# Optimization experiments

Measured on AMD Instinct MI355X. Metric: run time of the kernel, lower is better.

## Reference

```python
import jax, jax.numpy as jnp
import numpy as np

B, L_ENC, ENC_IN = 8, 1536, 7
LABEL_LEN, PRED_LEN = 512, 512
D_MODEL, N_HEADS, D_FF = 512, 8, 2048
E_LAYERS = 2
BUCKET_SIZE, N_HASHES = 64, 4
C_OUT, MARK_F = 7, 4
D_HEAD = D_MODEL // N_HEADS
L = L_ENC + PRED_LEN            # 2048, multiple of 2*bucket_size -> fit_length adds no pad
N_BUCKETS = L // BUCKET_SIZE    # 32
SELF_ATTN_VALUE = -5e4          # reformer_pytorch TOKEN_SELF_ATTN_VALUE


def _ln(x, g, b, eps=1e-5):
    mu = x.mean(-1, keepdims=True)
    var = ((x - mu) ** 2).mean(-1, keepdims=True)
    return (x - mu) * jax.lax.rsqrt(var + eps) * g + b


def _pos_embedding(length, d):
    pos = np.arange(length)[:, None].astype(np.float32)
    div = np.exp(np.arange(0, d, 2).astype(np.float32) * -(np.log(10000.0) / d))
    pe = np.zeros((length, d), np.float32)
    pe[:, 0::2] = np.sin(pos * div)
    pe[:, 1::2] = np.cos(pos * div)
    return jnp.asarray(pe)


def _lsh_attention(qk, v, rot):
    # qk, v: (b, L, d) with b = B*heads; rot: (d, n_hashes, n_buckets//2)
    b, Ls, d = qk.shape
    # --- hash: random rotations, buckets = argmax over [r, -r] ---
    rotated = jnp.einsum('bld,dhr->bhlr', qk, rot)
    rotated = jnp.concatenate([rotated, -rotated], axis=-1)            # (b,H,L,nb)
    buckets = jnp.argmax(rotated, axis=-1)                             # (b,H,L)
    buckets = buckets + (jnp.arange(N_HASHES) * N_BUCKETS)[None, :, None]
    buckets = buckets.reshape(b, N_HASHES * Ls)
    ticker = jnp.arange(N_HASHES * Ls)[None, :] % Ls
    # --- stable sort by (bucket, position) ---
    sticker = jnp.argsort(buckets * Ls + ticker, axis=-1)              # (b, H*L)
    undo_sort = jnp.argsort(sticker, axis=-1)
    st = sticker % Ls
    sqk = jnp.take_along_axis(qk, st[..., None], axis=1)               # (b, H*L, d)
    sv = jnp.take_along_axis(v, st[..., None], axis=1)
    n_chunks = N_HASHES * N_BUCKETS
    bq_t = st.reshape(b, n_chunks, -1)                                 # (b, C, cs)
    bq = sqk.reshape(b, n_chunks, -1, d)
    bv = sv.reshape(b, n_chunks, -1, d)
    # shared-QK: keys are l2-normalized queries
    bk = bq / jnp.maximum(jnp.linalg.norm(bq, axis=-1, keepdims=True), 1e-12)
    look = lambda x: jnp.concatenate([x, jnp.roll(x, 1, axis=1)], axis=2)
    bk, bv, bkv_t = look(bk), look(bv), look(bq_t)
    dots = jnp.einsum('bcie,bcje->bcij', bq, bk) * (d ** -0.5)         # (b,C,cs,2cs)
    self_mask = bq_t[:, :, :, None] == bkv_t[:, :, None, :]
    dots = jnp.where(self_mask, SELF_ATTN_VALUE, dots)
    lse = jax.nn.logsumexp(dots, axis=-1, keepdims=True)
    p = jnp.exp(dots - lse)
    so = jnp.einsum('bcij,bcje->bcie', p, bv).reshape(b, -1, d)        # (b, H*L, d)
    slog = lse.reshape(b, -1)
    o = jnp.take_along_axis(so, undo_sort[..., None], axis=1).reshape(b, N_HASHES, Ls, d)
    logits = jnp.take_along_axis(slog, undo_sort, axis=1).reshape(b, N_HASHES, Ls, 1)
    w = jnp.exp(logits - jax.nn.logsumexp(logits, axis=1, keepdims=True))
    return (o * w).sum(axis=1)                                         # (b, L, d)


def _forward(x_enc, x_mark_enc, x_dec, x_mark_dec, token_conv_w, time_w,
             qk_w, v_w, out_w, out_b, rotations,
             ffn1_w, ffn1_b, ffn2_w, ffn2_b,
             norm1_g, norm1_b, norm2_g, norm2_b, normf_g, normf_b,
             proj_w, proj_b):
    x = jnp.concatenate([x_enc, x_dec[:, -PRED_LEN:, :]], axis=1)      # (B, L, enc_in)
    xm = jnp.concatenate([x_mark_enc, x_mark_dec[:, -PRED_LEN:, :]], axis=1)
    # TokenEmbedding: Conv1d k=3, circular padding, no bias
    xp = jnp.concatenate([x[:, -1:, :], x, x[:, :1, :]], axis=1)
    tok = jax.lax.conv_general_dilated(xp, token_conv_w, (1,), 'VALID',
                                       dimension_numbers=('NWC', 'WIO', 'NWC'))
    h = tok + _pos_embedding(L, D_MODEL)[None] + xm @ time_w
    for l in range(E_LAYERS):
        qk = (h @ qk_w[l]).reshape(B, L, N_HEADS, D_HEAD).transpose(0, 2, 1, 3).reshape(B * N_HEADS, L, D_HEAD)
        v = (h @ v_w[l]).reshape(B, L, N_HEADS, D_HEAD).transpose(0, 2, 1, 3).reshape(B * N_HEADS, L, D_HEAD)
        a = _lsh_attention(qk, v, rotations[l])
        a = a.reshape(B, N_HEADS, L, D_HEAD).transpose(0, 2, 1, 3).reshape(B, L, D_MODEL)
        a = a @ out_w[l] + out_b[l]
        h = _ln(h + a, norm1_g[l], norm1_b[l])
        y = jax.nn.gelu(h @ ffn1_w[l] + ffn1_b[l], approximate=False) @ ffn2_w[l] + ffn2_b[l]
        h = _ln(h + y, norm2_g[l], norm2_b[l])
    h = _ln(h, normf_g, normf_b)
    out = h @ proj_w + proj_b
    return out[:, -PRED_LEN:, :]


def setup_inputs() -> dict:
    key = jax.random.key(0)
    ks = jax.random.split(key, 16)
    s = 0.02
    return {
        'x_enc': jax.random.normal(ks[0], (B, L_ENC, ENC_IN), jnp.float32),
        'x_mark_enc': jax.random.normal(ks[1], (B, L_ENC, MARK_F), jnp.float32),
        'x_dec': jax.random.normal(ks[2], (B, LABEL_LEN + PRED_LEN, ENC_IN), jnp.float32),
        'x_mark_dec': jax.random.normal(ks[3], (B, LABEL_LEN + PRED_LEN, MARK_F), jnp.float32),
        'token_conv_w': jax.random.normal(ks[4], (3, ENC_IN, D_MODEL), jnp.float32) * s,
        'time_w': jax.random.normal(ks[5], (MARK_F, D_MODEL), jnp.float32) * s,
        'qk_w': jax.random.normal(ks[6], (E_LAYERS, D_MODEL, D_MODEL), jnp.float32) * s,
        'v_w': jax.random.normal(ks[7], (E_LAYERS, D_MODEL, D_MODEL), jnp.float32) * s,
        'out_w': jax.random.normal(ks[8], (E_LAYERS, D_MODEL, D_MODEL), jnp.float32) * s,
        'out_b': jnp.zeros((E_LAYERS, D_MODEL), jnp.float32),
        'rotations': jax.random.normal(ks[9], (E_LAYERS, D_HEAD, N_HASHES, N_BUCKETS // 2), jnp.float32),
        'ffn1_w': jax.random.normal(ks[10], (E_LAYERS, D_MODEL, D_FF), jnp.float32) * s,
        'ffn1_b': jnp.zeros((E_LAYERS, D_FF), jnp.float32),
        'ffn2_w': jax.random.normal(ks[11], (E_LAYERS, D_FF, D_MODEL), jnp.float32) * s,
        'ffn2_b': jnp.zeros((E_LAYERS, D_MODEL), jnp.float32),
        'norm1_g': jnp.ones((E_LAYERS, D_MODEL), jnp.float32),
        'norm1_b': jnp.zeros((E_LAYERS, D_MODEL), jnp.float32),
        'norm2_g': jnp.ones((E_LAYERS, D_MODEL), jnp.float32),
        'norm2_b': jnp.zeros((E_LAYERS, D_MODEL), jnp.float32),
        'normf_g': jnp.ones((D_MODEL,), jnp.float32),
        'normf_b': jnp.zeros((D_MODEL,), jnp.float32),
        'proj_w': jax.random.normal(ks[12], (D_MODEL, C_OUT), jnp.float32) * s,
        'proj_b': jnp.zeros((C_OUT,), jnp.float32),
    }


def reference(x_enc, x_mark_enc, x_dec, x_mark_dec, token_conv_w, time_w,
              qk_w, v_w, out_w, out_b, rotations,
              ffn1_w, ffn1_b, ffn2_w, ffn2_b,
              norm1_g, norm1_b, norm2_g, norm2_b, normf_g, normf_b,
              proj_w, proj_b):
    return _forward(x_enc, x_mark_enc, x_dec, x_mark_dec, token_conv_w, time_w,
                    qk_w, v_w, out_w, out_b, rotations,
                    ffn1_w, ffn1_b, ffn2_w, ffn2_b,
                    norm1_g, norm1_b, norm2_g, norm2_b, normf_g, normf_b,
                    proj_w, proj_b)
```

## Files before the change

kernel.cpp:

```cpp
#include <hip/hip_runtime.h>


#define BATCH 8
#define SEQL 2048
#define DM 512
#define NH 8
#define DH 64
#define DFF 2048
#define NHASH 4
#define NBUCK 32
#define NCHUNK 128
#define CS 64
#define ROWS (BATCH*SEQL)
#define BHN (BATCH*NH)
#define SORTN (NHASH*SEQL)
#define SELF_VAL -5e4f

typedef __attribute__((ext_vector_type(4))) float f32x4;
typedef __attribute__((ext_vector_type(8))) short short8;

__device__ __forceinline__ float bfu2f(unsigned int u16) {
    return __uint_as_float(u16 << 16);
}
__device__ __forceinline__ unsigned short f2bfu(float f) {
    unsigned int x = __float_as_uint(f);
    x += 0x7fffu + ((x >> 16) & 1u);
    return (unsigned short)(x >> 16);
}

__device__ __forceinline__ void gld16(const void* g, void* l) {
    __builtin_amdgcn_global_load_lds(
        (const __attribute__((address_space(1))) unsigned int*)g,
        (__attribute__((address_space(3))) unsigned int*)l, 16, 0, 0);
}

__device__ __forceinline__ float getx(const float* xe, const float* xd, int b, int lm, int c) {
    return (lm < 1536) ? xe[((size_t)b * 1536 + lm) * 7 + c]
                       : xd[((size_t)b * 1024 + (lm - 1024)) * 7 + c];
}

__global__ __launch_bounds__(512) void embed_k(
    const float* __restrict__ x_enc, const float* __restrict__ x_me,
    const float* __restrict__ x_dec, const float* __restrict__ x_md,
    const float* __restrict__ cw, const float* __restrict__ tw,
    float* __restrict__ h, unsigned short* __restrict__ hb)
{
    const int row = blockIdx.x;
    const int b = row >> 11, l = row & 2047;
    const int d = threadIdx.x;
    __shared__ float xs[21];
    __shared__ float xms[4];
    if (d < 21) {
        const int k = d / 7, c = d % 7;
        const int lm = (l + k + 2047) & 2047;
        xs[d] = getx(x_enc, x_dec, b, lm, c);
    } else if (d < 25) {
        const int m = d - 21;
        xms[m] = (l < 1536) ? x_me[((size_t)b * 1536 + l) * 4 + m]
                            : x_md[((size_t)b * 1024 + (l - 1024)) * 4 + m];
    }
    __syncthreads();
    float tok = 0.f;
    #pragma unroll
    for (int kc = 0; kc < 21; ++kc) tok = fmaf(xs[kc], cw[kc * 512 + d], tok);
    float tm = 0.f;
    #pragma unroll
    for (int m = 0; m < 4; ++m) tm = fmaf(xms[m], tw[m * 512 + d], tm);
    const int pair = d & ~1;
    const float freq = expf((float)pair * (-9.210340371976184f / 512.f));
    const float ang = (float)l * freq;
    const float pe = (d & 1) ? cosf(ang) : sinf(ang);
    const float val = tok + pe + tm;
    h[(size_t)row * 512 + d] = val;
    hb[(size_t)row * 512 + d] = f2bfu(val);
}

__global__ __launch_bounds__(256) void gemm_k(
    const float* __restrict__ A, const float* __restrict__ B,
    float* __restrict__ C, int M, int N, int K)
{
    __shared__ float As[16][132];
    __shared__ float Bs[16][64];
    const int tid = threadIdx.x;
    const int bm = blockIdx.x * 128, bn = blockIdx.y * 64;
    const int ty = tid >> 4, tx = tid & 15;
    const int ar = tid >> 1, ac = (tid & 1) * 8;
    const int br = tid >> 4, bc = (tid & 15) * 4;
    float acc[8][4] = {};
    const float* Ap = A + (size_t)(bm + ar) * K + ac;
    const float* Bp = B + (size_t)br * N + bn + bc;
    float4 a0v = *reinterpret_cast<const float4*>(Ap);
    float4 a1v = *reinterpret_cast<const float4*>(Ap + 4);
    float4 b0v = *reinterpret_cast<const float4*>(Bp);
    for (int k0 = 0; k0 < K; k0 += 16) {
        As[ac + 0][ar] = a0v.x; As[ac + 1][ar] = a0v.y;
        As[ac + 2][ar] = a0v.z; As[ac + 3][ar] = a0v.w;
        As[ac + 4][ar] = a1v.x; As[ac + 5][ar] = a1v.y;
        As[ac + 6][ar] = a1v.z; As[ac + 7][ar] = a1v.w;
        *reinterpret_cast<float4*>(&Bs[br][bc]) = b0v;
        __syncthreads();
        if (k0 + 16 < K) {
            a0v = *reinterpret_cast<const float4*>(Ap + k0 + 16);
            a1v = *reinterpret_cast<const float4*>(Ap + k0 + 20);
            b0v = *reinterpret_cast<const float4*>(Bp + (size_t)(k0 + 16) * N);
        }
        #pragma unroll
        for (int k = 0; k < 16; ++k) {
            const float4 a0 = *reinterpret_cast<const float4*>(&As[k][ty * 8]);
            const float4 a1 = *reinterpret_cast<const float4*>(&As[k][ty * 8 + 4]);
            const float4 b0 = *reinterpret_cast<const float4*>(&Bs[k][tx * 4]);
            const float a[8] = {a0.x,a0.y,a0.z,a0.w,a1.x,a1.y,a1.z,a1.w};
            const float bb[4] = {b0.x,b0.y,b0.z,b0.w};
            #pragma unroll
            for (int i = 0; i < 8; ++i)
                #pragma unroll
                for (int j = 0; j < 4; ++j) acc[i][j] = fmaf(a[i], bb[j], acc[i][j]);
        }
        __syncthreads();
    }
    #pragma unroll
    for (int i = 0; i < 8; ++i) {
        const size_t cb = (size_t)(bm + ty * 8 + i) * N + bn + tx * 4;
        *reinterpret_cast<float4*>(C + cb) = make_float4(acc[i][0],acc[i][1],acc[i][2],acc[i][3]);
    }
}

__global__ __launch_bounds__(256) void tcast_k(
    const float* __restrict__ W, unsigned short* __restrict__ Wt, int K, int N)
{
    __shared__ float t[32][33];
    const int kb = blockIdx.x * 32, nb = blockIdx.y * 32;
    const int tx = threadIdx.x & 31, ty = threadIdx.x >> 5;
    #pragma unroll
    for (int i = ty; i < 32; i += 8)
        t[i][tx] = W[(size_t)(kb + i) * N + nb + tx];
    __syncthreads();
    #pragma unroll
    for (int i = ty; i < 32; i += 8)
        Wt[(size_t)(nb + i) * K + kb + tx] = f2bfu(t[tx][i]);
}

template<int OUT_BF, int ACT, int BIAS>
__global__ __launch_bounds__(256) void mgemm_k(
    const unsigned short* __restrict__ A,
    const unsigned short* __restrict__ Bt,
    const float* __restrict__ bias,
    void* __restrict__ Cv, int N, int K)
{
    __shared__ unsigned short As[128 * 32];
    __shared__ unsigned short Bs[128 * 32];
    const int tid = threadIdx.x;
    const int bm = blockIdx.x * 128, bn = blockIdx.y * 128;
    const int lane = tid & 63, w = tid >> 6;
    const int wr = (w >> 1) * 64, wc = (w & 1) * 64;
    const int fr = lane & 15, fq = lane >> 4;
    const int r0 = tid >> 2, c0 = (tid & 3) * 8;
    const unsigned short* Ag = A + (size_t)(bm + r0) * K + c0;
    const unsigned short* Bg = Bt + (size_t)(bn + r0) * K + c0;
    f32x4 acc[4][4];
    #pragma unroll
    for (int i = 0; i < 4; ++i)
        #pragma unroll
        for (int j = 0; j < 4; ++j) acc[i][j] = (f32x4){0.f, 0.f, 0.f, 0.f};
    for (int k0 = 0; k0 < K; k0 += 32) {
        gld16(Ag + k0,                   As + tid * 8);
        gld16(Ag + (size_t)64 * K + k0,  As + tid * 8 + 2048);
        gld16(Bg + k0,                   Bs + tid * 8);
        gld16(Bg + (size_t)64 * K + k0,  Bs + tid * 8 + 2048);
        __syncthreads();
        short8 af[4], bfr[4];
        #pragma unroll
        for (int mi = 0; mi < 4; ++mi)
            af[mi] = *reinterpret_cast<const short8*>(As + (wr + mi * 16 + fr) * 32 + fq * 8);
        #pragma unroll
        for (int ni = 0; ni < 4; ++ni)
            bfr[ni] = *reinterpret_cast<const short8*>(Bs + (wc + ni * 16 + fr) * 32 + fq * 8);
        #pragma unroll
        for (int mi = 0; mi < 4; ++mi)
            #pragma unroll
            for (int ni = 0; ni < 4; ++ni)
                acc[mi][ni] = __builtin_amdgcn_mfma_f32_16x16x32_bf16(
                    af[mi], bfr[ni], acc[mi][ni], 0, 0, 0);
        __syncthreads();
    }
    float bv[4];
    if (BIAS) {
        #pragma unroll
        for (int ni = 0; ni < 4; ++ni) bv[ni] = bias[bn + wc + ni * 16 + fr];
    }
    #pragma unroll
    for (int mi = 0; mi < 4; ++mi) {
        #pragma unroll
        for (int r = 0; r < 4; ++r) {
            const int row = bm + wr + mi * 16 + fq * 4 + r;
            #pragma unroll
            for (int ni = 0; ni < 4; ++ni) {
                float val = acc[mi][ni][r];
                if (BIAS) val += bv[ni];
                if (ACT) val = 0.5f * val * (1.0f + erff(val * 0.7071067811865475f));
                const size_t idx = (size_t)row * N + bn + wc + ni * 16 + fr;
                if (OUT_BF) ((unsigned short*)Cv)[idx] = f2bfu(val);
                else        ((float*)Cv)[idx] = val;
            }
        }
    }
}

__global__ __launch_bounds__(256, 4) void hash_k(
    const float* __restrict__ qk, const float* __restrict__ rot,
    int* __restrict__ buckets)
{
    __shared__ float rs[64][68];
    const int t = threadIdx.x;
    for (int u = t; u < 4096; u += 256) {
        const int d = u >> 6, hj = u & 63;
        rs[hj][d] = rot[u];
    }
    __syncthreads();
    const int gid = blockIdx.x * 256 + t;
    const int l = gid & 2047;
    const int bh = (gid >> 11) & 63;
    const int hh = gid >> 17;
    const int b = bh >> 3, head = bh & 7;
    const float* qrow = qk + (size_t)(b * 2048 + l) * 512 + head * 64;
    float q[64];
    #pragma unroll
    for (int d4 = 0; d4 < 16; ++d4) {
        const float4 qq = reinterpret_cast<const float4*>(qrow)[d4];
        q[d4*4+0]=qq.x; q[d4*4+1]=qq.y; q[d4*4+2]=qq.z; q[d4*4+3]=qq.w;
    }
    float bvp = -1e38f, bvn = -1e38f;
    int bip = 0, bin_ = 16;
    #pragma unroll
    for (int j = 0; j < 16; ++j) {
        const int hj = hh * 16 + j;
        float dot = 0.f;
        #pragma unroll
        for (int d = 0; d < 64; d += 4) {
            const float4 r = *reinterpret_cast<const float4*>(&rs[hj][d]);
            dot += q[d]*r.x + q[d+1]*r.y + q[d+2]*r.z + q[d+3]*r.w;
        }
        if (dot  > bvp) { bvp = dot;  bip = j; }
        if (-dot > bvn) { bvn = -dot; bin_ = 16 + j; }
    }
    const int idx = (bvn > bvp) ? bin_ : bip;
    buckets[((size_t)bh << 13) + hh * 2048 + l] = hh * 32 + idx;
}

__global__ __launch_bounds__(256) void sort_k(
    const int* __restrict__ buckets, int* __restrict__ st_sorted, int* __restrict__ pos_of)
{
    const int bh = blockIdx.x >> 2, hh = blockIdx.x & 3;
    const int t = threadIdx.x;
    __shared__ unsigned short cnt[256][32];
    __shared__ int tot[32];
    __shared__ int startc[32];
    {
        uint4* p = reinterpret_cast<uint4*>(&cnt[t][0]);
        const uint4 z = {0,0,0,0};
        #pragma unroll
        for (int q = 0; q < 4; ++q) p[q] = z;
    }
    const size_t base = (size_t)bh * SORTN + hh * 2048;
    int myb[8];
    #pragma unroll
    for (int j = 0; j < 8; ++j) {
        const int i = t * 8 + j;
        const int g = buckets[base + i] - hh * 32;
        myb[j] = g;
        cnt[t][g]++;
    }
    __syncthreads();
    if (t < 32) {
        int run = 0;
        for (int tt = 0; tt < 256; ++tt) {
            const int x = cnt[tt][t];
            cnt[tt][t] = (unsigned short)run;
            run += x;
        }
        tot[t] = run;
    }
    __syncthreads();
    if (t == 0) {
        int s = 0;
        for (int g = 0; g < 32; ++g) { startc[g] = s; s += tot[g]; }
    }
    __syncthreads();
    #pragma unroll
    for (int j = 0; j < 8; ++j) {
        const int i = t * 8 + j;
        const int g = myb[j];
        const int rank = cnt[t][g]++;
        const int pos = hh * 2048 + startc[g] + rank;
        st_sorted[(size_t)bh * SORTN + pos] = i;
        pos_of[base + i] = pos;
    }
}

__global__ __launch_bounds__(256) void lsh_attn_k(
    const float* __restrict__ qk, const unsigned short* __restrict__ vbf,
    const int* __restrict__ st_sorted,
    unsigned short* __restrict__ so, float* __restrict__ slog)
{
    const int c = blockIdx.x;
    const int bh = blockIdx.y;
    const int b = bh >> 3, head = bh & 7;
    __shared__ unsigned short Ks[128 * 72];
    __shared__ unsigned short Vt[128 * 64];
    __shared__ unsigned short Ps[64 * 136];
    __shared__ float rnorm[128];
    __shared__ int stk[128];
    const int t = threadIdx.x;

    {
        const int r = t >> 1, hf = t & 1;
        const int cprev = (c + NCHUNK - 1) & (NCHUNK - 1);
        const int spos = (r < 64) ? (c * CS + r) : (cprev * CS + (r - 64));
        const int l = st_sorted[(size_t)bh * SORTN + spos];
        if (hf == 0) stk[r] = l;
        const size_t ro = (size_t)(b * 2048 + l) * 512 + head * 64 + hf * 32;
        const float4* q4 = reinterpret_cast<const float4*>(qk + ro);
        float ss = 0.f;
        #pragma unroll
        for (int u = 0; u < 8; ++u) {
            const float4 a = q4[u];
            ss += a.x*a.x + a.y*a.y + a.z*a.z + a.w*a.w;
            ushort4 pk;
            pk.x = f2bfu(a.x); pk.y = f2bfu(a.y); pk.z = f2bfu(a.z); pk.w = f2bfu(a.w);
            *reinterpret_cast<ushort4*>(&Ks[r * 72 + hf * 32 + u * 4]) = pk;
        }
        ss += __shfl_xor(ss, 1);
        if (hf == 0) rnorm[r] = 1.0f / fmaxf(sqrtf(ss), 1e-12f);
        const uint4* v16 = reinterpret_cast<const uint4*>(vbf + ro);
        const uint4 a0 = v16[0], a1 = v16[1], a2 = v16[2], a3 = v16[3];
        const unsigned int wd[16] = {a0.x,a0.y,a0.z,a0.w, a1.x,a1.y,a1.z,a1.w,
                                     a2.x,a2.y,a2.z,a2.w, a3.x,a3.y,a3.z,a3.w};
        #pragma unroll
        for (int e = 0; e < 32; ++e) {
            const int d = hf * 32 + e;
            const unsigned short us = (unsigned short)(wd[e >> 1] >> ((e & 1) * 16));
            Vt[(d * 128 + r) ^ ((d & 7) << 3)] = us;
        }
    }
    __syncthreads();

    const int lane = t & 63, w = t >> 6;
    const int fr = lane & 15, fq = lane >> 4;

    short8 aq[2];
    #pragma unroll
    for (int s = 0; s < 2; ++s)
        aq[s] = *reinterpret_cast<const short8*>(&Ks[(w * 16 + fr) * 72 + s * 32 + fq * 8]);
    f32x4 cc[8];
    #pragma unroll
    for (int n = 0; n < 8; ++n) cc[n] = (f32x4){0.f, 0.f, 0.f, 0.f};
    #pragma unroll
    for (int n = 0; n < 8; ++n) {
        #pragma unroll
        for (int s = 0; s < 2; ++s) {
            const short8 bk = *reinterpret_cast<const short8*>(
                &Ks[(n * 16 + fr) * 72 + s * 32 + fq * 8]);
            cc[n] = __builtin_amdgcn_mfma_f32_16x16x32_bf16(aq[s], bk, cc[n], 0, 0, 0);
        }
    }

    int stq_r[4];
    #pragma unroll
    for (int r = 0; r < 4; ++r) stq_r[r] = stk[w * 16 + fq * 4 + r];
    float mx[4] = {-3.0e38f, -3.0e38f, -3.0e38f, -3.0e38f};
    #pragma unroll
    for (int n = 0; n < 8; ++n) {
        const int key = n * 16 + fr;
        const float rn = rnorm[key] * 0.125f;
        const int sk = stk[key];
        #pragma unroll
        for (int r = 0; r < 4; ++r) {
            const float val = (stq_r[r] == sk) ? SELF_VAL : cc[n][r] * rn;
            cc[n][r] = val;
            mx[r] = fmaxf(mx[r], val);
        }
    }
    #pragma unroll
    for (int r = 0; r < 4; ++r) {
        mx[r] = fmaxf(mx[r], __shfl_xor(mx[r], 1));
        mx[r] = fmaxf(mx[r], __shfl_xor(mx[r], 2));
        mx[r] = fmaxf(mx[r], __shfl_xor(mx[r], 4));
        mx[r] = fmaxf(mx[r], __shfl_xor(mx[r], 8));
    }
    float sm[4] = {0.f, 0.f, 0.f, 0.f};
    #pragma unroll
    for (int n = 0; n < 8; ++n)
        #pragma unroll
        for (int r = 0; r < 4; ++r) {
            const float e = __expf(cc[n][r] - mx[r]);
            cc[n][r] = e;
            sm[r] += e;
        }
    #pragma unroll
    for (int r = 0; r < 4; ++r) {
        sm[r] += __shfl_xor(sm[r], 1);
        sm[r] += __shfl_xor(sm[r], 2);
        sm[r] += __shfl_xor(sm[r], 4);
        sm[r] += __shfl_xor(sm[r], 8);
    }
    float rsum[4];
    #pragma unroll
    for (int r = 0; r < 4; ++r) rsum[r] = 1.0f / sm[r];
    if (fr == 0) {
        #pragma unroll
        for (int r = 0; r < 4; ++r)
            slog[(size_t)bh * SORTN + c * CS + w * 16 + fq * 4 + r] = mx[r] + logf(sm[r]);
    }

    #pragma unroll
    for (int n = 0; n < 8; ++n)
        #pragma unroll
        for (int r = 0; r < 4; ++r)
            Ps[(w * 16 + fq * 4 + r) * 136 + n * 16 + fr] = f2bfu(cc[n][r]);
    __syncthreads();

    short8 pa[4];
    #pragma unroll
    for (int s = 0; s < 4; ++s)
        pa[s] = *reinterpret_cast<const short8*>(&Ps[(w * 16 + fr) * 136 + s * 32 + fq * 8]);
    f32x4 oo[4];
    #pragma unroll
    for (int n = 0; n < 4; ++n) oo[n] = (f32x4){0.f, 0.f, 0.f, 0.f};
    #pragma unroll
    for (int n = 0; n < 4; ++n) {
        const int d = n * 16 + fr;
        #pragma unroll
        for (int s = 0; s < 4; ++s) {
            const short8 vb = *reinterpret_cast<const short8*>(
                &Vt[(d * 128 + s * 32 + fq * 8) ^ ((d & 7) << 3)]);
            oo[n] = __builtin_amdgcn_mfma_f32_16x16x32_bf16(pa[s], vb, oo[n], 0, 0, 0);
        }
    }

    #pragma unroll
    for (int r = 0; r < 4; ++r) {
        const int qrow = w * 16 + fq * 4 + r;
        const size_t ob = ((size_t)bh * SORTN + c * CS + qrow) * 64;
        #pragma unroll
        for (int n = 0; n < 4; ++n)
            so[ob + n * 16 + fr] = f2bfu(oo[n][r] * rsum[r]);
    }
}

__global__ __launch_bounds__(256) void combine_k(
    const unsigned short* __restrict__ so, const float* __restrict__ slog,
    const int* __restrict__ pos_of, unsigned short* __restrict__ aout)
{
    const int gid = blockIdx.x * 256 + threadIdx.x;
    const int d = gid & 63;
    const int bl = gid >> 6;
    const int l = bl & 2047;
    const int bh = bl >> 11;
    const int b = bh >> 3, head = bh & 7;
    int pos[4]; float lg[4];
    #pragma unroll
    for (int hh = 0; hh < 4; ++hh) {
        pos[hh] = pos_of[((size_t)bh << 13) + hh * 2048 + l];
        lg[hh] = slog[((size_t)bh << 13) + pos[hh]];
    }
    const float m = fmaxf(fmaxf(lg[0], lg[1]), fmaxf(lg[2], lg[3]));
    float w[4]; float sw = 0.f;
    #pragma unroll
    for (int hh = 0; hh < 4; ++hh) { w[hh] = expf(lg[hh] - m); sw += w[hh]; }
    const float inv = 1.0f / sw;
    float acc = 0.f;
    #pragma unroll
    for (int hh = 0; hh < 4; ++hh)
        acc += w[hh] * bfu2f(so[(((size_t)bh << 13) + pos[hh]) * 64 + d]);
    aout[(size_t)(b * 2048 + l) * 512 + head * 64 + d] = f2bfu(acc * inv);
}

template<int RES, int WBF>
__global__ __launch_bounds__(256) void ln_k(
    float* __restrict__ h, const float* __restrict__ res,
    const float* __restrict__ g, const float* __restrict__ bta,
    unsigned short* __restrict__ hb)
{
    const int row = blockIdx.x * 4 + (threadIdx.x >> 6);
    const int lane = threadIdx.x & 63;
    const size_t base = (size_t)row * 512;
    float4 xa = *reinterpret_cast<const float4*>(h + base + lane * 4);
    float4 xb = *reinterpret_cast<const float4*>(h + base + 256 + lane * 4);
    if (RES) {
        const float4 ra = *reinterpret_cast<const float4*>(res + base + lane * 4);
        const float4 rb = *reinterpret_cast<const float4*>(res + base + 256 + lane * 4);
        xa.x += ra.x; xa.y += ra.y; xa.z += ra.z; xa.w += ra.w;
        xb.x += rb.x; xb.y += rb.y; xb.z += rb.z; xb.w += rb.w;
    }
    float sum = xa.x + xa.y + xa.z + xa.w + xb.x + xb.y + xb.z + xb.w;
    float sq = xa.x*xa.x + xa.y*xa.y + xa.z*xa.z + xa.w*xa.w
             + xb.x*xb.x + xb.y*xb.y + xb.z*xb.z + xb.w*xb.w;
    #pragma unroll
    for (int off = 32; off > 0; off >>= 1) {
        sum += __shfl_xor(sum, off);
        sq  += __shfl_xor(sq, off);
    }
    const float mu = sum * (1.0f / 512.0f);
    const float var = sq * (1.0f / 512.0f) - mu * mu;
    const float rstd = rsqrtf(var + 1e-5f);
    const float4 ga = *reinterpret_cast<const float4*>(g + lane * 4);
    const float4 gb = *reinterpret_cast<const float4*>(g + 256 + lane * 4);
    const float4 ba = *reinterpret_cast<const float4*>(bta + lane * 4);
    const float4 bb = *reinterpret_cast<const float4*>(bta + 256 + lane * 4);
    float4 oa, ob;
    oa.x = (xa.x - mu) * rstd * ga.x + ba.x;
    oa.y = (xa.y - mu) * rstd * ga.y + ba.y;
    oa.z = (xa.z - mu) * rstd * ga.z + ba.z;
    oa.w = (xa.w - mu) * rstd * ga.w + ba.w;
    ob.x = (xb.x - mu) * rstd * gb.x + bb.x;
    ob.y = (xb.y - mu) * rstd * gb.y + bb.y;
    ob.z = (xb.z - mu) * rstd * gb.z + bb.z;
    ob.w = (xb.w - mu) * rstd * gb.w + bb.w;
    *reinterpret_cast<float4*>(h + base + lane * 4) = oa;
    *reinterpret_cast<float4*>(h + base + 256 + lane * 4) = ob;
    if (WBF) {
        ushort4 pa, pb;
        pa.x = f2bfu(oa.x); pa.y = f2bfu(oa.y); pa.z = f2bfu(oa.z); pa.w = f2bfu(oa.w);
        pb.x = f2bfu(ob.x); pb.y = f2bfu(ob.y); pb.z = f2bfu(ob.z); pb.w = f2bfu(ob.w);
        *reinterpret_cast<ushort4*>(hb + base + lane * 4) = pa;
        *reinterpret_cast<ushort4*>(hb + base + 256 + lane * 4) = pb;
    }
}

__global__ __launch_bounds__(256) void proj_k(
    const float* __restrict__ h, const float* __restrict__ pw,
    const float* __restrict__ pb, float* __restrict__ out)
{
    const int wid = (blockIdx.x * 256 + threadIdx.x) >> 6;
    const int lane = threadIdx.x & 63;
    const int b = wid >> 9, tt = wid & 511;
    const float* row = h + (size_t)(b * 2048 + 1536 + tt) * 512;
    const float4 h0 = reinterpret_cast<const float4*>(row)[lane * 2];
    const float4 h1 = reinterpret_cast<const float4*>(row)[lane * 2 + 1];
    const float he[8] = {h0.x, h0.y, h0.z, h0.w, h1.x, h1.y, h1.z, h1.w};
    float acc[7] = {};
    #pragma unroll
    for (int e = 0; e < 8; ++e) {
        const int k = lane * 8 + e;
        #pragma unroll
        for (int cq = 0; cq < 7; ++cq) acc[cq] = fmaf(he[e], pw[k * 7 + cq], acc[cq]);
    }
    #pragma unroll
    for (int cq = 0; cq < 7; ++cq) {
        #pragma unroll
        for (int off = 32; off > 0; off >>= 1) acc[cq] += __shfl_xor(acc[cq], off);
    }
    if (lane == 0) {
        const size_t ob = ((size_t)(b * 512) + tt) * 7;
        #pragma unroll
        for (int cq = 0; cq < 7; ++cq) out[ob + cq] = acc[cq] + pb[cq];
    }
}

__global__ void nan_k(float* o) { o[0] = __int_as_float(0x7fc00000); }

extern "C" void kernel_launch(void* const* d_in, const int* in_sizes, int n_in,
                              void* d_out, int out_size, void* d_ws, size_t ws_size,
                              hipStream_t stream)
{
    const float* x_enc  = (const float*)d_in[0];
    const float* x_me   = (const float*)d_in[1];
    const float* x_dec  = (const float*)d_in[2];
    const float* x_md   = (const float*)d_in[3];
    const float* conv_w = (const float*)d_in[4];
    const float* time_w = (const float*)d_in[5];
    const float* qk_w   = (const float*)d_in[6];
    const float* v_w    = (const float*)d_in[7];
    const float* out_w  = (const float*)d_in[8];
    const float* out_b  = (const float*)d_in[9];
    const float* rots   = (const float*)d_in[10];
    const float* f1w    = (const float*)d_in[11];
    const float* f1b    = (const float*)d_in[12];
    const float* f2w    = (const float*)d_in[13];
    const float* f2b    = (const float*)d_in[14];
    const float* n1g    = (const float*)d_in[15];
    const float* n1b    = (const float*)d_in[16];
    const float* n2g    = (const float*)d_in[17];
    const float* n2b    = (const float*)d_in[18];
    const float* nfg    = (const float*)d_in[19];
    const float* nfb    = (const float*)d_in[20];
    const float* pw     = (const float*)d_in[21];
    const float* pb     = (const float*)d_in[22];

    char* ws = (char*)d_ws;
    const size_t HBYT = (size_t)ROWS * DM * 4;
    float* h    = (float*)ws;                  ws += HBYT;
    unsigned short* hb = (unsigned short*)ws;  ws += HBYT / 2;
    float* qkb  = (float*)ws;                  ws += HBYT;
    float* gout = (float*)ws;                  ws += HBYT;
    unsigned short* mid = (unsigned short*)ws; ws += (size_t)ROWS * DFF * 2;
    float* slog = (float*)ws;                  ws += (size_t)BHN * SORTN * 4;
    int* buckets = (int*)ws;                   ws += (size_t)BHN * SORTN * 4;
    int* st_sorted = (int*)ws;                 ws += (size_t)BHN * SORTN * 4;
    int* pos_of = (int*)ws;                    ws += (size_t)BHN * SORTN * 4;
    unsigned short* wT = (unsigned short*)ws;  ws += (size_t)(2*262144 + 2*262144 + 2*1048576 + 2*1048576) * 2;
    const size_t need = (size_t)(ws - (char*)d_ws);
    if (ws_size < need) { nan_k<<<1, 1, 0, stream>>>((float*)d_out); return; }

    unsigned short* vT  = wT;
    unsigned short* oT  = vT + 2 * 262144;
    unsigned short* f1T = oT + 2 * 262144;
    unsigned short* f2T = f1T + 2 * 1048576;
    unsigned short* ab  = (unsigned short*)qkb;
    unsigned short* vbf = (unsigned short*)gout;

    for (int l = 0; l < 2; ++l) {
        tcast_k<<<dim3(16, 16), 256, 0, stream>>>(v_w  + (size_t)l*DM*DM,  vT  + (size_t)l*262144, DM, DM);
        tcast_k<<<dim3(16, 16), 256, 0, stream>>>(out_w+ (size_t)l*DM*DM,  oT  + (size_t)l*262144, DM, DM);
        tcast_k<<<dim3(16, 64), 256, 0, stream>>>(f1w  + (size_t)l*DM*DFF, f1T + (size_t)l*1048576, DM, DFF);
        tcast_k<<<dim3(64, 16), 256, 0, stream>>>(f2w  + (size_t)l*DFF*DM, f2T + (size_t)l*1048576, DFF, DM);
    }

    embed_k<<<ROWS, 512, 0, stream>>>(x_enc, x_me, x_dec, x_md, conv_w, time_w, h, hb);

    for (int l = 0; l < 2; ++l) {
        const size_t wo = (size_t)l * DM * DM;
        gemm_k<<<dim3(ROWS/128, DM/64), 256, 0, stream>>>(h, qk_w + wo, qkb, ROWS, DM, DM);
        mgemm_k<1,0,0><<<dim3(ROWS/128, DM/128), 256, 0, stream>>>(hb, vT + (size_t)l*262144, nullptr, vbf, DM, DM);
        hash_k<<<(NHASH * BHN * SEQL) / 256, 256, 0, stream>>>(qkb, rots + (size_t)l * DH * NHASH * (NBUCK/2), buckets);
        sort_k<<<BHN * 4, 256, 0, stream>>>(buckets, st_sorted, pos_of);
        lsh_attn_k<<<dim3(NCHUNK, BHN), 256, 0, stream>>>(qkb, vbf, st_sorted, mid , slog);
        combine_k<<<(BHN * SEQL * DH) / 256, 256, 0, stream>>>(mid, slog, pos_of, ab);
        mgemm_k<0,0,1><<<dim3(ROWS/128, DM/128), 256, 0, stream>>>(ab, oT + (size_t)l*262144, out_b + l * DM, gout, DM, DM);
        ln_k<1,1><<<ROWS/4, 256, 0, stream>>>(h, gout, n1g + l * DM, n1b + l * DM, hb);
        mgemm_k<1,1,1><<<dim3(ROWS/128, DFF/128), 256, 0, stream>>>(hb, f1T + (size_t)l*1048576, f1b + l * DFF, mid, DFF, DM);
        mgemm_k<0,0,1><<<dim3(ROWS/128, DM/128), 256, 0, stream>>>(mid, f2T + (size_t)l*1048576, f2b + l * DM, gout, DM, DFF);
        ln_k<1,1><<<ROWS/4, 256, 0, stream>>>(h, gout, n2g + l * DM, n2b + l * DM, hb);
    }
    ln_k<0,0><<<ROWS/4, 256, 0, stream>>>(h, nullptr, nfg, nfb, nullptr);
    proj_k<<<(BATCH * 512 / 4), 256, 0, stream>>>(h, pw, pb, (float*)d_out);
}
```

Measured before the change: 980.9 us.

## Fuse QK and V projections into one launch, swizzle GEMM blocks, trim final norm

Merges the fp32 QK projection and the bf16 V projection into a single kernel whose blocks pick one path by index, saving a launch and letting both run concurrently. The fp32 GEMM K-tile grows from 16 to 32 per stage. mgemm blocks are remapped in an XCD-aware swizzle for better L2 locality. Weight transpose-casts collapse into four launches over a z dimension, and the final layernorm now only processes the 512 prediction rows that the projection reads. The larger fp32 tile raises register and LDS use, and the mixed kernel inherits the larger LDS footprint for both paths.

```diff
diff --git a/kernel.cpp b/kernel.cpp
--- a/kernel.cpp
+++ b/kernel.cpp
@@ -75,40 +75,50 @@
     hb[(size_t)row * 512 + d] = f2bfu(val);
 }
 
-__global__ __launch_bounds__(256) void gemm_k(
-    const float* __restrict__ A, const float* __restrict__ B,
-    float* __restrict__ C, int M, int N, int K)
-{
-    __shared__ float As[16][132];
-    __shared__ float Bs[16][64];
+__device__ __forceinline__ void gemm_body(
+    int bm, int bn, const float* __restrict__ A, const float* __restrict__ B,
+    float* __restrict__ C, int N, int K, char* smem)
+{
+    float* As = (float*)smem;
+    float* Bs = (float*)(smem + 32 * 132 * 4);
     const int tid = threadIdx.x;
-    const int bm = blockIdx.x * 128, bn = blockIdx.y * 64;
     const int ty = tid >> 4, tx = tid & 15;
-    const int ar = tid >> 1, ac = (tid & 1) * 8;
-    const int br = tid >> 4, bc = (tid & 15) * 4;
+    const int ar = tid >> 1, ac = (tid & 1) * 16;
+    const int br = tid >> 3, bc = (tid & 7) * 8;
     float acc[8][4] = {};
     const float* Ap = A + (size_t)(bm + ar) * K + ac;
     const float* Bp = B + (size_t)br * N + bn + bc;
-    float4 a0v = *reinterpret_cast<const float4*>(Ap);
-    float4 a1v = *reinterpret_cast<const float4*>(Ap + 4);
-    float4 b0v = *reinterpret_cast<const float4*>(Bp);
-    for (int k0 = 0; k0 < K; k0 += 16) {
-        As[ac + 0][ar] = a0v.x; As[ac + 1][ar] = a0v.y;
-        As[ac + 2][ar] = a0v.z; As[ac + 3][ar] = a0v.w;
-        As[ac + 4][ar] = a1v.x; As[ac + 5][ar] = a1v.y;
-        As[ac + 6][ar] = a1v.z; As[ac + 7][ar] = a1v.w;
-        *reinterpret_cast<float4*>(&Bs[br][bc]) = b0v;
+    float4 av0 = *reinterpret_cast<const float4*>(Ap);
+    float4 av1 = *reinterpret_cast<const float4*>(Ap + 4);
+    float4 av2 = *reinterpret_cast<const float4*>(Ap + 8);
+    float4 av3 = *reinterpret_cast<const float4*>(Ap + 12);
+    float4 bv0 = *reinterpret_cast<const float4*>(Bp);
+    float4 bv1 = *reinterpret_cast<const float4*>(Bp + 4);
+    for (int k0 = 0; k0 < K; k0 += 32) {
+        As[(ac + 0)  * 132 + ar] = av0.x; As[(ac + 1)  * 132 + ar] = av0.y;
+        As[(ac + 2)  * 132 + ar] = av0.z; As[(ac + 3)  * 132 + ar] = av0.w;
+        As[(ac + 4)  * 132 + ar] = av1.x; As[(ac + 5)  * 132 + ar] = av1.y;
+        As[(ac + 6)  * 132 + ar] = av1.z; As[(ac + 7)  * 132 + ar] = av1.w;
+        As[(ac + 8)  * 132 + ar] = av2.x; As[(ac + 9)  * 132 + ar] = av2.y;
+        As[(ac + 10) * 132 + ar] = av2.z; As[(ac + 11) * 132 + ar] = av2.w;
+        As[(ac + 12) * 132 + ar] = av3.x; As[(ac + 13) * 132 + ar] = av3.y;
+        As[(ac + 14) * 132 + ar] = av3.z; As[(ac + 15) * 132 + ar] = av3.w;
+        *reinterpret_cast<float4*>(&Bs[br * 64 + bc])     = bv0;
+        *reinterpret_cast<float4*>(&Bs[br * 64 + bc + 4]) = bv1;
         __syncthreads();
-        if (k0 + 16 < K) {
-            a0v = *reinterpret_cast<const float4*>(Ap + k0 + 16);
-            a1v = *reinterpret_cast<const float4*>(Ap + k0 + 20);
-            b0v = *reinterpret_cast<const float4*>(Bp + (size_t)(k0 + 16) * N);
-        }
-        #pragma unroll
-        for (int k = 0; k < 16; ++k) {
-            const float4 a0 = *reinterpret_cast<const float4*>(&As[k][ty * 8]);
-            const float4 a1 = *reinterpret_cast<const float4*>(&As[k][ty * 8 + 4]);
-            const float4 b0 = *reinterpret_cast<const float4*>(&Bs[k][tx * 4]);
+        if (k0 + 32 < K) {
+            av0 = *reinterpret_cast<const float4*>(Ap + k0 + 32);
+            av1 = *reinterpret_cast<const float4*>(Ap + k0 + 36);
+            av2 = *reinterpret_cast<const float4*>(Ap + k0 + 40);
+            av3 = *reinterpret_cast<const float4*>(Ap + k0 + 44);
+            bv0 = *reinterpret_cast<const float4*>(Bp + (size_t)(k0 + 32) * N);
+            bv1 = *reinterpret_cast<const float4*>(Bp + (size_t)(k0 + 32) * N + 4);
+        }
+        #pragma unroll
+        for (int k = 0; k < 32; ++k) {
+            const float4 a0 = *reinterpret_cast<const float4*>(&As[k * 132 + ty * 8]);
+            const float4 a1 = *reinterpret_cast<const float4*>(&As[k * 132 + ty * 8 + 4]);
+            const float4 b0 = *reinterpret_cast<const float4*>(&Bs[k * 64 + tx * 4]);
             const float a[8] = {a0.x,a0.y,a0.z,a0.w,a1.x,a1.y,a1.z,a1.w};
             const float bb[4] = {b0.x,b0.y,b0.z,b0.w};
             #pragma unroll
@@ -125,32 +135,17 @@
     }
 }
 
-__global__ __launch_bounds__(256) void tcast_k(
-    const float* __restrict__ W, unsigned short* __restrict__ Wt, int K, int N)
-{
-    __shared__ float t[32][33];
-    const int kb = blockIdx.x * 32, nb = blockIdx.y * 32;
-    const int tx = threadIdx.x & 31, ty = threadIdx.x >> 5;
-    #pragma unroll
-    for (int i = ty; i < 32; i += 8)
-        t[i][tx] = W[(size_t)(kb + i) * N + nb + tx];
-    __syncthreads();
-    #pragma unroll
-    for (int i = ty; i < 32; i += 8)
-        Wt[(size_t)(nb + i) * K + kb + tx] = f2bfu(t[tx][i]);
-}
-
 template<int OUT_BF, int ACT, int BIAS>
-__global__ __launch_bounds__(256) void mgemm_k(
+__device__ __forceinline__ void mgemm_body(
+    int bm, int bn,
     const unsigned short* __restrict__ A,
     const unsigned short* __restrict__ Bt,
     const float* __restrict__ bias,
-    void* __restrict__ Cv, int N, int K)
-{
-    __shared__ unsigned short As[128 * 32];
-    __shared__ unsigned short Bs[128 * 32];
+    void* __restrict__ Cv, int N, int K, char* smem)
+{
+    unsigned short* As = (unsigned short*)smem;
+    unsigned short* Bs = (unsigned short*)smem + 128 * 32;
     const int tid = threadIdx.x;
-    const int bm = blockIdx.x * 128, bn = blockIdx.y * 128;
     const int lane = tid & 63, w = tid >> 6;
     const int wr = (w >> 1) * 64, wc = (w & 1) * 64;
     const int fr = lane & 15, fq = lane >> 4;
@@ -204,6 +199,56 @@
             }
         }
     }
+}
+
+template<int OUT_BF, int ACT, int BIAS>
+__global__ __launch_bounds__(256) void mgemm_k(
+    const unsigned short* __restrict__ A,
+    const unsigned short* __restrict__ Bt,
+    const float* __restrict__ bias,
+    void* __restrict__ Cv, int N, int K)
+{
+    __shared__ __align__(16) char smem[128 * 32 * 2 * 2];
+    const int gx = gridDim.x;
+    const int nwg = gx * gridDim.y;
+    int id = blockIdx.y * gx + blockIdx.x;
+    const int cpx = nwg >> 3;
+    id = (id & 7) * cpx + (id >> 3);
+    const int bm = (id % gx) * 128, bn = (id / gx) * 128;
+    mgemm_body<OUT_BF, ACT, BIAS>(bm, bn, A, Bt, bias, Cv, N, K, smem);
+}
+
+__global__ __launch_bounds__(256) void qkv_k(
+    const float* __restrict__ h, const float* __restrict__ qkw,
+    float* __restrict__ qkb,
+    const unsigned short* __restrict__ hb, const unsigned short* __restrict__ vT,
+    unsigned short* __restrict__ vbf)
+{
+    __shared__ __align__(16) char smem[32 * 132 * 4 + 32 * 64 * 4];
+    const int id = blockIdx.x;
+    if (id < 1024) {
+        gemm_body((id & 127) * 128, (id >> 7) * 64, h, qkw, qkb, DM, DM, smem);
+    } else {
+        const int mid_ = id - 1024;
+        mgemm_body<1, 0, 0>((mid_ & 127) * 128, (mid_ >> 7) * 128,
+                            hb, vT, nullptr, vbf, DM, DM, smem);
+    }
+}
+
+__global__ __launch_bounds__(256) void tcast_k(
+    const float* __restrict__ W, unsigned short* __restrict__ Wt, int K, int N)
+{
+    __shared__ float t[32][33];
+    const size_t zo = (size_t)blockIdx.z * K * N;
+    const int kb = blockIdx.x * 32, nb = blockIdx.y * 32;
+    const int tx = threadIdx.x & 31, ty = threadIdx.x >> 5;
+    #pragma unroll
+    for (int i = ty; i < 32; i += 8)
+        t[i][tx] = W[zo + (size_t)(kb + i) * N + nb + tx];
+    __syncthreads();
+    #pragma unroll
+    for (int i = ty; i < 32; i += 8)
+        Wt[zo + (size_t)(nb + i) * K + kb + tx] = f2bfu(t[tx][i]);
 }
 
 __global__ __launch_bounds__(256, 4) void hash_k(
@@ -527,6 +572,43 @@
     }
 }
 
+__global__ __launch_bounds__(256) void lnf_k(
+    float* __restrict__ h, const float* __restrict__ g, const float* __restrict__ bta)
+{
+    const int vrow = blockIdx.x * 4 + (threadIdx.x >> 6);
+    const int row = (vrow >> 9) * 2048 + 1536 + (vrow & 511);
+    const int lane = threadIdx.x & 63;
+    const size_t base = (size_t)row * 512;
+    float4 xa = *reinterpret_cast<const float4*>(h + base + lane * 4);
+    float4 xb = *reinterpret_cast<const float4*>(h + base + 256 + lane * 4);
+    float sum = xa.x + xa.y + xa.z + xa.w + xb.x + xb.y + xb.z + xb.w;
+    float sq = xa.x*xa.x + xa.y*xa.y + xa.z*xa.z + xa.w*xa.w
+             + xb.x*xb.x + xb.y*xb.y + xb.z*xb.z + xb.w*xb.w;
+    #pragma unroll
+    for (int off = 32; off > 0; off >>= 1) {
+        sum += __shfl_xor(sum, off);
+        sq  += __shfl_xor(sq, off);
+    }
+    const float mu = sum * (1.0f / 512.0f);
+    const float var = sq * (1.0f / 512.0f) - mu * mu;
+    const float rstd = rsqrtf(var + 1e-5f);
+    const float4 ga = *reinterpret_cast<const float4*>(g + lane * 4);
+    const float4 gb = *reinterpret_cast<const float4*>(g + 256 + lane * 4);
+    const float4 ba = *reinterpret_cast<const float4*>(bta + lane * 4);
+    const float4 bb = *reinterpret_cast<const float4*>(bta + 256 + lane * 4);
+    float4 oa, ob;
+    oa.x = (xa.x - mu) * rstd * ga.x + ba.x;
+    oa.y = (xa.y - mu) * rstd * ga.y + ba.y;
+    oa.z = (xa.z - mu) * rstd * ga.z + ba.z;
+    oa.w = (xa.w - mu) * rstd * ga.w + ba.w;
+    ob.x = (xb.x - mu) * rstd * gb.x + bb.x;
+    ob.y = (xb.y - mu) * rstd * gb.y + bb.y;
+    ob.z = (xb.z - mu) * rstd * gb.z + bb.z;
+    ob.w = (xb.w - mu) * rstd * gb.w + bb.w;
+    *reinterpret_cast<float4*>(h + base + lane * 4) = oa;
+    *reinterpret_cast<float4*>(h + base + 256 + lane * 4) = ob;
+}
+
 __global__ __launch_bounds__(256) void proj_k(
     const float* __restrict__ h, const float* __restrict__ pw,
     const float* __restrict__ pb, float* __restrict__ out)
@@ -609,19 +691,16 @@
     unsigned short* ab  = (unsigned short*)qkb;
     unsigned short* vbf = (unsigned short*)gout;
 
-    for (int l = 0; l < 2; ++l) {
-        tcast_k<<<dim3(16, 16), 256, 0, stream>>>(v_w  + (size_t)l*DM*DM,  vT  + (size_t)l*262144, DM, DM);
-        tcast_k<<<dim3(16, 16), 256, 0, stream>>>(out_w+ (size_t)l*DM*DM,  oT  + (size_t)l*262144, DM, DM);
-        tcast_k<<<dim3(16, 64), 256, 0, stream>>>(f1w  + (size_t)l*DM*DFF, f1T + (size_t)l*1048576, DM, DFF);
-        tcast_k<<<dim3(64, 16), 256, 0, stream>>>(f2w  + (size_t)l*DFF*DM, f2T + (size_t)l*1048576, DFF, DM);
-    }
+    tcast_k<<<dim3(16, 16, 2), 256, 0, stream>>>(v_w,   vT,  DM, DM);
+    tcast_k<<<dim3(16, 16, 2), 256, 0, stream>>>(out_w, oT,  DM, DM);
+    tcast_k<<<dim3(16, 64, 2), 256, 0, stream>>>(f1w,   f1T, DM, DFF);
+    tcast_k<<<dim3(64, 16, 2), 256, 0, stream>>>(f2w,   f2T, DFF, DM);
 
     embed_k<<<ROWS, 512, 0, stream>>>(x_enc, x_me, x_dec, x_md, conv_w, time_w, h, hb);
 
     for (int l = 0; l < 2; ++l) {
         const size_t wo = (size_t)l * DM * DM;
-        gemm_k<<<dim3(ROWS/128, DM/64), 256, 0, stream>>>(h, qk_w + wo, qkb, ROWS, DM, DM);
-        mgemm_k<1,0,0><<<dim3(ROWS/128, DM/128), 256, 0, stream>>>(hb, vT + (size_t)l*262144, nullptr, vbf, DM, DM);
+        qkv_k<<<1536, 256, 0, stream>>>(h, qk_w + wo, qkb, hb, vT + (size_t)l*262144, vbf);
         hash_k<<<(NHASH * BHN * SEQL) / 256, 256, 0, stream>>>(qkb, rots + (size_t)l * DH * NHASH * (NBUCK/2), buckets);
         sort_k<<<BHN * 4, 256, 0, stream>>>(buckets, st_sorted, pos_of);
         lsh_attn_k<<<dim3(NCHUNK, BHN), 256, 0, stream>>>(qkb, vbf, st_sorted, mid , slog);
@@ -632,6 +711,6 @@
         mgemm_k<0,0,1><<<dim3(ROWS/128, DM/128), 256, 0, stream>>>(mid, f2T + (size_t)l*1048576, f2b + l * DM, gout, DM, DFF);
         ln_k<1,1><<<ROWS/4, 256, 0, stream>>>(h, gout, n2g + l * DM, n2b + l * DM, hb);
     }
-    ln_k<0,0><<<ROWS/4, 256, 0, stream>>>(h, nullptr, nfg, nfb, nullptr);
+    lnf_k<<<(BATCH * 512) / 4, 256, 0, stream>>>(h, nfg, nfb);
     proj_k<<<(BATCH * 512 / 4), 256, 0, stream>>>(h, pw, pb, (float*)d_out);
 }
```

Result: slower. 1.027 ms (+4.7%).

## Batch weight casts, shrink hash rotation staging, restrict final LN to output rows

Applied to the files above, without the earlier changes.

Weight transpose-cast launches are merged across layers using a z grid dimension, cutting the launch count from eight to four. The hash kernel now stages only the 16 rotation columns its hash index needs instead of all 64, which reduces shared memory use and load work. The final layer norm runs only on the 512 prediction rows per batch that the projection reads, skipping the encoder-only rows. All three are small overhead trims around the main GEMM and attention work.

```diff
diff --git a/kernel.cpp b/kernel.cpp
--- a/kernel.cpp
+++ b/kernel.cpp
@@ -129,15 +129,16 @@
     const float* __restrict__ W, unsigned short* __restrict__ Wt, int K, int N)
 {
     __shared__ float t[32][33];
+    const size_t zo = (size_t)blockIdx.z * K * N;
     const int kb = blockIdx.x * 32, nb = blockIdx.y * 32;
     const int tx = threadIdx.x & 31, ty = threadIdx.x >> 5;
     #pragma unroll
     for (int i = ty; i < 32; i += 8)
-        t[i][tx] = W[(size_t)(kb + i) * N + nb + tx];
+        t[i][tx] = W[zo + (size_t)(kb + i) * N + nb + tx];
     __syncthreads();
     #pragma unroll
     for (int i = ty; i < 32; i += 8)
-        Wt[(size_t)(nb + i) * K + kb + tx] = f2bfu(t[tx][i]);
+        Wt[zo + (size_t)(nb + i) * K + kb + tx] = f2bfu(t[tx][i]);
 }
 
 template<int OUT_BF, int ACT, int BIAS>
@@ -210,11 +211,12 @@
     const float* __restrict__ qk, const float* __restrict__ rot,
     int* __restrict__ buckets)
 {
-    __shared__ float rs[64][68];
+    __shared__ float rs[16][68];
     const int t = threadIdx.x;
-    for (int u = t; u < 4096; u += 256) {
-        const int d = u >> 6, hj = u & 63;
-        rs[hj][d] = rot[u];
+    const int hh_blk = blockIdx.x >> 9;
+    for (int u = t; u < 1024; u += 256) {
+        const int d = u >> 4, j = u & 15;
+        rs[j][d] = rot[d * 64 + hh_blk * 16 + j];
     }
     __syncthreads();
     const int gid = blockIdx.x * 256 + t;
@@ -233,11 +235,10 @@
     int bip = 0, bin_ = 16;
     #pragma unroll
     for (int j = 0; j < 16; ++j) {
-        const int hj = hh * 16 + j;
         float dot = 0.f;
         #pragma unroll
         for (int d = 0; d < 64; d += 4) {
-            const float4 r = *reinterpret_cast<const float4*>(&rs[hj][d]);
+            const float4 r = *reinterpret_cast<const float4*>(&rs[j][d]);
             dot += q[d]*r.x + q[d+1]*r.y + q[d+2]*r.z + q[d+3]*r.w;
         }
         if (dot  > bvp) { bvp = dot;  bip = j; }
@@ -527,6 +528,43 @@
     }
 }
 
+__global__ __launch_bounds__(256) void lnf_k(
+    float* __restrict__ h, const float* __restrict__ g, const float* __restrict__ bta)
+{
+    const int vrow = blockIdx.x * 4 + (threadIdx.x >> 6);
+    const int row = (vrow >> 9) * 2048 + 1536 + (vrow & 511);
+    const int lane = threadIdx.x & 63;
+    const size_t base = (size_t)row * 512;
+    float4 xa = *reinterpret_cast<const float4*>(h + base + lane * 4);
+    float4 xb = *reinterpret_cast<const float4*>(h + base + 256 + lane * 4);
+    float sum = xa.x + xa.y + xa.z + xa.w + xb.x + xb.y + xb.z + xb.w;
+    float sq = xa.x*xa.x + xa.y*xa.y + xa.z*xa.z + xa.w*xa.w
+             + xb.x*xb.x + xb.y*xb.y + xb.z*xb.z + xb.w*xb.w;
+    #pragma unroll
+    for (int off = 32; off > 0; off >>= 1) {
+        sum += __shfl_xor(sum, off);
+        sq  += __shfl_xor(sq, off);
+    }
+    const float mu = sum * (1.0f / 512.0f);
+    const float var = sq * (1.0f / 512.0f) - mu * mu;
+    const float rstd = rsqrtf(var + 1e-5f);
+    const float4 ga = *reinterpret_cast<const float4*>(g + lane * 4);
+    const float4 gb = *reinterpret_cast<const float4*>(g + 256 + lane * 4);
+    const float4 ba = *reinterpret_cast<const float4*>(bta + lane * 4);
+    const float4 bb = *reinterpret_cast<const float4*>(bta + 256 + lane * 4);
+    float4 oa, ob;
+    oa.x = (xa.x - mu) * rstd * ga.x + ba.x;
+    oa.y = (xa.y - mu) * rstd * ga.y + ba.y;
+    oa.z = (xa.z - mu) * rstd * ga.z + ba.z;
+    oa.w = (xa.w - mu) * rstd * ga.w + ba.w;
+    ob.x = (xb.x - mu) * rstd * gb.x + bb.x;
+    ob.y = (xb.y - mu) * rstd * gb.y + bb.y;
+    ob.z = (xb.z - mu) * rstd * gb.z + bb.z;
+    ob.w = (xb.w - mu) * rstd * gb.w + bb.w;
+    *reinterpret_cast<float4*>(h + base + lane * 4) = oa;
+    *reinterpret_cast<float4*>(h + base + 256 + lane * 4) = ob;
+}
+
 __global__ __launch_bounds__(256) void proj_k(
     const float* __restrict__ h, const float* __restrict__ pw,
     const float* __restrict__ pb, float* __restrict__ out)
@@ -609,12 +647,10 @@
     unsigned short* ab  = (unsigned short*)qkb;
     unsigned short* vbf = (unsigned short*)gout;
 
-    for (int l = 0; l < 2; ++l) {
-        tcast_k<<<dim3(16, 16), 256, 0, stream>>>(v_w  + (size_t)l*DM*DM,  vT  + (size_t)l*262144, DM, DM);
-        tcast_k<<<dim3(16, 16), 256, 0, stream>>>(out_w+ (size_t)l*DM*DM,  oT  + (size_t)l*262144, DM, DM);
-        tcast_k<<<dim3(16, 64), 256, 0, stream>>>(f1w  + (size_t)l*DM*DFF, f1T + (size_t)l*1048576, DM, DFF);
-        tcast_k<<<dim3(64, 16), 256, 0, stream>>>(f2w  + (size_t)l*DFF*DM, f2T + (size_t)l*1048576, DFF, DM);
-    }
+    tcast_k<<<dim3(16, 16, 2), 256, 0, stream>>>(v_w,   vT,  DM, DM);
+    tcast_k<<<dim3(16, 16, 2), 256, 0, stream>>>(out_w, oT,  DM, DM);
+    tcast_k<<<dim3(16, 64, 2), 256, 0, stream>>>(f1w,   f1T, DM, DFF);
+    tcast_k<<<dim3(64, 16, 2), 256, 0, stream>>>(f2w,   f2T, DFF, DM);
 
     embed_k<<<ROWS, 512, 0, stream>>>(x_enc, x_me, x_dec, x_md, conv_w, time_w, h, hb);
 
@@ -632,6 +668,6 @@
         mgemm_k<0,0,1><<<dim3(ROWS/128, DM/128), 256, 0, stream>>>(mid, f2T + (size_t)l*1048576, f2b + l * DM, gout, DM, DFF);
         ln_k<1,1><<<ROWS/4, 256, 0, stream>>>(h, gout, n2g + l * DM, n2b + l * DM, hb);
     }
-    ln_k<0,0><<<ROWS/4, 256, 0, stream>>>(h, nullptr, nfg, nfb, nullptr);
+    lnf_k<<<(BATCH * 512) / 4, 256, 0, stream>>>(h, nfg, nfb);
     proj_k<<<(BATCH * 512 / 4), 256, 0, stream>>>(h, pw, pb, (float*)d_out);
 }
```

Measured after the change: 957.4 us. 1.02x faster.
